# Performance work log

Hardware: AMD Instinct MI355X
Metric: run time of the kernel (lower is better)

## Reference

```python
import jax, jax.numpy as jnp
import numpy as np
import math

DIM = 1536; NH = 12; HD = 128
F, H, W = 6, 30, 30
S = F * H * W
B = 1
K_LEN = 9900  # hardcoded k_lens in the source forward
EPS_NORM = 1e-6


def _rope_tables(max_len=1024, d=HD):
    # Wan rope_params: three tables of widths d-4*(d//6), 2*(d//6), 2*(d//6)
    # -> cos/sin tables of half-widths 22, 21, 21 (concat = d//2 = 64)
    def ang(dd):
        inv = 1.0 / (10000.0 ** (np.arange(0, dd, 2, dtype=np.float64) / dd))
        return np.outer(np.arange(max_len, dtype=np.float64), inv)
    a = np.concatenate([ang(d - 4 * (d // 6)), ang(2 * (d // 6)), ang(2 * (d // 6))], axis=1)
    return np.cos(a).astype(np.float32), np.sin(a).astype(np.float32)


def setup_inputs() -> dict:
    key = jax.random.key(0)
    ks = jax.random.split(key, 5)
    s = 1.0 / math.sqrt(DIM)
    cos, sin = _rope_tables()
    return {
        "x": jax.random.normal(ks[0], (B, S, DIM), jnp.float32),
        "q_w": jax.random.normal(ks[1], (DIM, DIM), jnp.float32) * s,
        "q_b": jnp.zeros((DIM,), jnp.float32),
        "k_w": jax.random.normal(ks[2], (DIM, DIM), jnp.float32) * s,
        "k_b": jnp.zeros((DIM,), jnp.float32),
        "v_w": jax.random.normal(ks[3], (DIM, DIM), jnp.float32) * s,
        "v_b": jnp.zeros((DIM,), jnp.float32),
        "o_w": jax.random.normal(ks[4], (DIM, DIM), jnp.float32) * s,
        "o_b": jnp.zeros((DIM,), jnp.float32),
        "norm_q_w": jnp.ones((DIM,), jnp.float32),
        "norm_k_w": jnp.ones((DIM,), jnp.float32),
        "freqs_cos": jnp.asarray(cos),
        "freqs_sin": jnp.asarray(sin),
        "grid_f": F, "grid_h": H, "grid_w": W,
    }


def rms_norm(x, w):
    # RMSNorm over full model dim, computed in fp32 (as in source)
    xf = x.astype(jnp.float32)
    xn = xf * jax.lax.rsqrt(jnp.mean(xf * xf, axis=-1, keepdims=True) + EPS_NORM)
    return xn.astype(x.dtype) * w


def rope_apply(x, cos, sin, f, h, w):
    # x: [B,S,N,D]; rotate consecutive pairs with 3D-factorized (f,h,w) freqs
    Bb, Ss, Nn, Dd = x.shape
    c = Dd // 2
    sp = [c - 2 * (c // 3), c // 3, c // 3]  # 22, 21, 21

    def grid(tab):
        tf = tab[:, :sp[0]]
        th = tab[:, sp[0]:sp[0] + sp[1]]
        tw = tab[:, sp[0] + sp[1]:]
        g = jnp.concatenate([
            jnp.broadcast_to(tf[:f, None, None, :], (f, h, w, sp[0])),
            jnp.broadcast_to(th[None, :h, None, :], (f, h, w, sp[1])),
            jnp.broadcast_to(tw[None, None, :w, :], (f, h, w, sp[2])),
        ], axis=-1)
        return g.reshape(f * h * w, 1, c)  # [S,1,c] (broadcast over heads)

    gc, gs = grid(cos), grid(sin)
    xp = x.astype(jnp.float32).reshape(Bb, Ss, Nn, c, 2)
    xr, xi = xp[..., 0], xp[..., 1]
    orr = xr * gc - xi * gs
    oii = xr * gs + xi * gc
    return jnp.stack([orr, oii], axis=-1).reshape(Bb, Ss, Nn, Dd).astype(x.dtype)


def attention(q, k, v, k_len):
    # full attention (window_size=(-1,-1)) with keys masked beyond k_len
    scale = 1.0 / math.sqrt(q.shape[-1])
    att = jnp.einsum('bqnd,bknd->bnqk', q, k) * scale
    valid = jnp.arange(k.shape[1]) < k_len
    att = jnp.where(valid[None, None, None, :], att, jnp.finfo(att.dtype).min)
    p = jax.nn.softmax(att, axis=-1)
    return jnp.einsum('bnqk,bknd->bqnd', p, v)


def reference(x, q_w, q_b, k_w, k_b, v_w, v_b, o_w, o_b, norm_q_w, norm_k_w, freqs_cos, freqs_sin, grid_f, grid_h, grid_w):
    Bb, Ss, _ = x.shape
    q = rms_norm(x @ q_w.T + q_b, norm_q_w).reshape(Bb, Ss, NH, HD)
    k = rms_norm(x @ k_w.T + k_b, norm_k_w).reshape(Bb, Ss, NH, HD)
    v = (x @ v_w.T + v_b).reshape(Bb, Ss, NH, HD)
    q = rope_apply(q, freqs_cos, freqs_sin, grid_f, grid_h, grid_w)
    k = rope_apply(k, freqs_cos, freqs_sin, grid_f, grid_h, grid_w)
    o = attention(q, k, v, K_LEN).reshape(Bb, Ss, NH * HD)
    return o @ o_w.T + o_b
```

## Files before the change

kernel.cpp:

```cpp
#include <hip/hip_runtime.h>

#define DIM 1536
#define NH 12
#define HD 128
#define S_LEN 5400
#define SPAD 5440
#define MPAD 5504
#define NQKV 4608
#define EPS_NORM 1e-6f

typedef __bf16 bf16_t;
typedef __bf16 bf16x8 __attribute__((ext_vector_type(8)));
typedef __bf16 bf16x4 __attribute__((ext_vector_type(4)));
typedef float  f32x4  __attribute__((ext_vector_type(4)));
typedef float  f32x16 __attribute__((ext_vector_type(16)));

#define GLOAD_LDS16(gp, lp) __builtin_amdgcn_global_load_lds( \
    (__attribute__((address_space(1))) void*)(void*)(gp),     \
    (__attribute__((address_space(3))) void*)(lp), 16, 0, 0)


__global__ __launch_bounds__(256) void cvt_x_kernel(const float* __restrict__ x,
                                                    bf16_t* __restrict__ xb) {
  size_t base = ((size_t)blockIdx.x * 256 + threadIdx.x) * 4;
  if (base >= (size_t)MPAD * DIM) return;
  size_t row = base / DIM;
  float4 v = make_float4(0.f, 0.f, 0.f, 0.f);
  if (row < S_LEN) v = *(const float4*)&x[base];
  bf16x4 o; o[0] = (__bf16)v.x; o[1] = (__bf16)v.y; o[2] = (__bf16)v.z; o[3] = (__bf16)v.w;
  *(bf16x4*)&xb[base] = o;
}

__global__ __launch_bounds__(256) void cvt_wqkv_kernel(const float* __restrict__ qw,
                                                       const float* __restrict__ kw,
                                                       const float* __restrict__ vw,
                                                       bf16_t* __restrict__ wb) {
  size_t base = ((size_t)blockIdx.x * 256 + threadIdx.x) * 4;
  if (base >= (size_t)NQKV * DIM) return;
  int row = (int)(base / DIM);
  int col = (int)(base - (size_t)row * DIM);
  const float* src; int rr = row;
  if (rr >= 3072)      { src = vw; rr -= 3072; }
  else if (rr >= 1536) { src = kw; rr -= 1536; }
  else                 { src = qw; }
  float4 v = *(const float4*)&src[(size_t)rr * DIM + col];
  bf16x4 o; o[0] = (__bf16)v.x; o[1] = (__bf16)v.y; o[2] = (__bf16)v.z; o[3] = (__bf16)v.w;
  *(bf16x4*)&wb[base] = o;
}

__global__ __launch_bounds__(256) void cvt_wo_kernel(const float* __restrict__ w,
                                                     bf16_t* __restrict__ wb) {
  size_t base = ((size_t)blockIdx.x * 256 + threadIdx.x) * 4;
  if (base >= (size_t)DIM * DIM) return;
  float4 v = *(const float4*)&w[base];
  bf16x4 o; o[0] = (__bf16)v.x; o[1] = (__bf16)v.y; o[2] = (__bf16)v.z; o[3] = (__bf16)v.w;
  *(bf16x4*)&wb[base] = o;
}


template<bool OUT_BF16>
__global__ __launch_bounds__(256) void gemm_bt_kernel(
    const bf16_t* __restrict__ A, const bf16_t* __restrict__ B, void* __restrict__ C,
    const float* __restrict__ bias0, const float* __restrict__ bias1,
    const float* __restrict__ bias2, int M, int N, int K, int Mvalid) {
  __shared__ bf16_t As[2][128 * 32];
  __shared__ bf16_t Bs[2][128 * 32];
  int tid = threadIdx.x;
  int lane = tid & 63, wave = tid >> 6, quad = lane >> 4, l16 = lane & 15;
  int m0 = blockIdx.y * 128, n0 = blockIdx.x * 128;
  int wm = (wave >> 1) * 64, wn = (wave & 1) * 64;
  const bf16_t* Ab = A + (size_t)m0 * K;
  const bf16_t* Bb = B + (size_t)n0 * K;
  f32x4 acc[4][4] = {};

  int eo0 = tid * 8;
  int row0 = eo0 >> 5, col0 = eo0 & 31;
  int eo1 = (256 + tid) * 8;
  int row1 = eo1 >> 5, col1 = eo1 & 31;

  GLOAD_LDS16(Ab + (size_t)row0 * K + col0, &As[0][eo0]);
  GLOAD_LDS16(Bb + (size_t)row0 * K + col0, &Bs[0][eo0]);
  GLOAD_LDS16(Ab + (size_t)row1 * K + col1, &As[0][eo1]);
  GLOAD_LDS16(Bb + (size_t)row1 * K + col1, &Bs[0][eo1]);
  asm volatile("s_waitcnt vmcnt(0)" ::: "memory");
  __builtin_amdgcn_s_barrier();
  __builtin_amdgcn_sched_barrier(0);

  int KT = K >> 5;
  for (int t = 0; t < KT; t++) {
    int cur = t & 1;
    if (t + 1 < KT) {
      int kn = (t + 1) << 5;
      GLOAD_LDS16(Ab + (size_t)row0 * K + kn + col0, &As[cur ^ 1][eo0]);
      GLOAD_LDS16(Bb + (size_t)row0 * K + kn + col0, &Bs[cur ^ 1][eo0]);
      GLOAD_LDS16(Ab + (size_t)row1 * K + kn + col1, &As[cur ^ 1][eo1]);
      GLOAD_LDS16(Bb + (size_t)row1 * K + kn + col1, &Bs[cur ^ 1][eo1]);
    }
    bf16x8 af[4], bfr[4];
#pragma unroll
    for (int i = 0; i < 4; i++)
      af[i] = *(const bf16x8*)&As[cur][(wm + i * 16 + l16) * 32 + quad * 8];
#pragma unroll
    for (int j = 0; j < 4; j++)
      bfr[j] = *(const bf16x8*)&Bs[cur][(wn + j * 16 + l16) * 32 + quad * 8];
#pragma unroll
    for (int i = 0; i < 4; i++)
#pragma unroll
      for (int j = 0; j < 4; j++)
        acc[i][j] = __builtin_amdgcn_mfma_f32_16x16x32_bf16(af[i], bfr[j], acc[i][j], 0, 0, 0);
    asm volatile("s_waitcnt vmcnt(0) lgkmcnt(0)" ::: "memory");
    __builtin_amdgcn_s_barrier();
    __builtin_amdgcn_sched_barrier(0);
  }
#pragma unroll
  for (int j = 0; j < 4; j++) {
    int n = n0 + wn + j * 16 + l16;
    float bias = (n < 1536) ? bias0[n] : (n < 3072) ? bias1[n - 1536] : bias2[n - 3072];
#pragma unroll
    for (int i = 0; i < 4; i++) {
#pragma unroll
      for (int r = 0; r < 4; r++) {
        int m = m0 + wm + i * 16 + quad * 4 + r;
        float v = acc[i][j][r] + bias;
        if (OUT_BF16) {
          ((bf16_t*)C)[(size_t)m * N + n] = (__bf16)v;
        } else {
          if (m < Mvalid) ((float*)C)[(size_t)m * N + n] = v;
        }
      }
    }
  }
}


__global__ __launch_bounds__(256) void rope_qk_kernel(
    const bf16_t* __restrict__ qkv, const float* __restrict__ nqw,
    const float* __restrict__ nkw, const float* __restrict__ fcos,
    const float* __restrict__ fsin, bf16_t* __restrict__ qout,
    bf16_t* __restrict__ kout) {
  int s = blockIdx.x;
  int tid = threadIdx.x;
  bool valid = s < S_LEN;
  int f = s / 900, hh = (s / 30) % 30, ww = s % 30;
  __shared__ float red[4];
  for (int which = 0; which < 2; which++) {
    const bf16_t* src = qkv + (size_t)s * NQKV + which * DIM;
    const float* nw = which ? nkw : nqw;
    bf16_t* dst = (which ? kout : qout) + (size_t)s * DIM;
    float osc = which ? 1.0f : 0.08838834764831845f;
    float v[6]; float ss = 0.f;
#pragma unroll
    for (int i = 0; i < 6; i++) {
      v[i] = valid ? (float)src[tid * 6 + i] : 0.f;
      ss += v[i] * v[i];
    }
#pragma unroll
    for (int off = 32; off >= 1; off >>= 1) ss += __shfl_down(ss, off);
    if ((tid & 63) == 0) red[tid >> 6] = ss;
    __syncthreads();
    float tot = red[0] + red[1] + red[2] + red[3];
    float rn = rsqrtf(tot * (1.f / DIM) + EPS_NORM);
    __syncthreads();
#pragma unroll
    for (int i = 0; i < 3; i++) {
      int e0 = tid * 6 + 2 * i;
      int p = e0 >> 1;
      int cc = p & 63;
      int pos = (cc < 22) ? f : (cc < 43) ? hh : ww;
      float c = fcos[pos * 64 + cc], sn = fsin[pos * 64 + cc];
      float xr = v[2 * i] * rn * nw[e0];
      float xi = v[2 * i + 1] * rn * nw[e0 + 1];
      dst[e0]     = (__bf16)((xr * c - xi * sn) * osc);
      dst[e0 + 1] = (__bf16)((xr * sn + xi * c) * osc);
    }
  }
}


__global__ __launch_bounds__(256) void v_transpose_kernel(const bf16_t* __restrict__ qkv,
                                                          bf16_t* __restrict__ vt) {
  __shared__ bf16_t tile[64][136];
  int h = blockIdx.y, s0 = blockIdx.x * 64, tid = threadIdx.x;
#pragma unroll
  for (int it = 0; it < 4; it++) {
    int eo = (it * 256 + tid) * 8;
    int row = eo >> 7, col = eo & 127;
    int s = s0 + row;
    bf16x8 val = {};
    if (s < S_LEN) val = *(const bf16x8*)&qkv[(size_t)s * NQKV + 3072 + h * HD + col];
    *(bf16x8*)&tile[row][col] = val;
  }
  __syncthreads();
  int d = tid & 127, j0 = (tid >> 7) * 32;
  bf16x8 outv[4];
#pragma unroll
  for (int b = 0; b < 4; b++)
#pragma unroll
    for (int j = 0; j < 8; j++) outv[b][j] = tile[j0 + b * 8 + j][d];
  size_t base = ((size_t)h * HD + d) * SPAD + s0 + j0;
#pragma unroll
  for (int b = 0; b < 4; b++) *(bf16x8*)&vt[base + b * 8] = outv[b];
}


__global__ __launch_bounds__(256, 2) void flash_attn_kernel(
    const bf16_t* __restrict__ q, const bf16_t* __restrict__ k,
    const bf16_t* __restrict__ vt, bf16_t* __restrict__ o) {
  __shared__ bf16_t Ks[2][64 * 128];
  __shared__ bf16_t Vs[2][64 * 128];
  __shared__ bf16_t Pw[4][32 * 64];
  int head = blockIdx.y;
  int s0 = blockIdx.x * 128;
  int tid = threadIdx.x, w = tid >> 6, lane = tid & 63;
  int l31 = lane & 31, hh = lane >> 5;

  bf16x8 bq[8];
  {
    const bf16_t* qp = &q[(size_t)(s0 + w * 32 + l31) * DIM + head * HD + hh * 8];
#pragma unroll
    for (int kc = 0; kc < 8; kc++) bq[kc] = *(const bf16x8*)(qp + kc * 16);
  }

  float m_i = -1e30f, l_i = 0.f;
  f32x16 oacc[4] = {};

  const int NT = SPAD / 64;

#pragma unroll
  for (int it = 0; it < 4; it++) {
    int slot = it * 256 + tid;
    int row = slot >> 4, pc = slot & 15;
    int c = pc ^ (row & 15);
    GLOAD_LDS16(k + (size_t)row * DIM + head * HD + c * 8, &Ks[0][slot * 8]);
  }
#pragma unroll
  for (int it = 0; it < 4; it++) {
    int slot = it * 256 + tid;
    int row = slot >> 4, pc = slot & 15;
    int cp = pc ^ (row & 15);
    int d = 2 * row + (cp >> 3);
    GLOAD_LDS16(vt + ((size_t)head * HD + d) * SPAD + (cp & 7) * 8, &Vs[0][slot * 8]);
  }
  asm volatile("s_waitcnt vmcnt(0)" ::: "memory");
  __builtin_amdgcn_s_barrier();
  __builtin_amdgcn_sched_barrier(0);

  for (int t = 0; t < NT; t++) {
    int kt = t * 64;
    int cur = t & 1;

    if (t + 1 < NT) {
      int kn = kt + 64;
#pragma unroll
      for (int it = 0; it < 4; it++) {
        int slot = it * 256 + tid;
        int row = slot >> 4, pc = slot & 15;
        int c = pc ^ (row & 15);
        GLOAD_LDS16(k + (size_t)(kn + row) * DIM + head * HD + c * 8, &Ks[cur ^ 1][slot * 8]);
      }
#pragma unroll
      for (int it = 0; it < 4; it++) {
        int slot = it * 256 + tid;
        int row = slot >> 4, pc = slot & 15;
        int cp = pc ^ (row & 15);
        int d = 2 * row + (cp >> 3);
        GLOAD_LDS16(vt + ((size_t)head * HD + d) * SPAD + kn + (cp & 7) * 8, &Vs[cur ^ 1][slot * 8]);
      }
    }

    f32x16 sacc[2] = {};
    __builtin_amdgcn_s_setprio(1);
#pragma unroll
    for (int ns = 0; ns < 2; ns++) {
      int row = ns * 32 + l31;
#pragma unroll
      for (int kc = 0; kc < 8; kc++) {
        int pc = (kc * 2 + hh) ^ (row & 15);
        bf16x8 ak = *(const bf16x8*)&Ks[cur][row * 128 + pc * 8];
        sacc[ns] = __builtin_amdgcn_mfma_f32_32x32x16_bf16(ak, bq[kc], sacc[ns], 0, 0, 0);
      }
    }
    __builtin_amdgcn_s_setprio(0);

    if (kt + 64 > S_LEN) {
#pragma unroll
      for (int ns = 0; ns < 2; ns++)
#pragma unroll
        for (int r = 0; r < 16; r++) {
          int kvg = kt + ns * 32 + (r & 3) + 8 * (r >> 2) + 4 * hh;
          if (kvg >= S_LEN) sacc[ns][r] = -1e30f;
        }
    }

    float mx = -1e30f;
#pragma unroll
    for (int ns = 0; ns < 2; ns++)
#pragma unroll
      for (int r = 0; r < 16; r++) mx = fmaxf(mx, sacc[ns][r]);
    mx = fmaxf(mx, __shfl_xor(mx, 32));
    if (!__all(mx - m_i <= 8.f)) {
      float mn = fmaxf(m_i, mx);
      float al = __expf(m_i - mn);
      l_i *= al;
#pragma unroll
      for (int dt = 0; dt < 4; dt++)
#pragma unroll
        for (int r = 0; r < 16; r++) oacc[dt][r] *= al;
      m_i = mn;
    }
    float rs = 0.f;
#pragma unroll
    for (int ns = 0; ns < 2; ns++)
#pragma unroll
      for (int r = 0; r < 16; r++) {
        float p = __expf(sacc[ns][r] - m_i);
        rs += p;
        sacc[ns][r] = p;
      }
    rs += __shfl_xor(rs, 32);
    l_i += rs;

#pragma unroll
    for (int ns = 0; ns < 2; ns++)
#pragma unroll
      for (int tt = 0; tt < 4; tt++) {
        bf16x4 pk;
#pragma unroll
        for (int r4 = 0; r4 < 4; r4++) pk[r4] = (__bf16)sacc[ns][tt * 4 + r4];
        int c8 = ns * 8 + 2 * tt + hh;
        int pc8 = c8 ^ (l31 & 15);
        *(bf16x4*)&Pw[w][l31 * 64 + pc8 * 4] = pk;
      }

    __builtin_amdgcn_s_setprio(1);
#pragma unroll
    for (int kvc = 0; kvc < 4; kvc++) {
      int c8a = kvc * 4 + hh * 2;
      bf16x4 plo = *(const bf16x4*)&Pw[w][l31 * 64 + ((c8a) ^ (l31 & 15)) * 4];
      bf16x4 phi = *(const bf16x4*)&Pw[w][l31 * 64 + ((c8a + 1) ^ (l31 & 15)) * 4];
      bf16x8 bp;
#pragma unroll
      for (int j = 0; j < 4; j++) { bp[j] = plo[j]; bp[j + 4] = phi[j]; }
#pragma unroll
      for (int dt = 0; dt < 4; dt++) {
        int d = dt * 32 + l31;
        int r = d >> 1;
        int cp = ((d & 1) << 3) | (kvc * 2 + hh);
        int pc = cp ^ (r & 15);
        bf16x8 av = *(const bf16x8*)&Vs[cur][r * 128 + pc * 8];
        oacc[dt] = __builtin_amdgcn_mfma_f32_32x32x16_bf16(av, bp, oacc[dt], 0, 0, 0);
      }
    }
    __builtin_amdgcn_s_setprio(0);

    asm volatile("s_waitcnt vmcnt(0) lgkmcnt(0)" ::: "memory");
    __builtin_amdgcn_s_barrier();
    __builtin_amdgcn_sched_barrier(0);
  }

  float inv = 1.f / l_i;
  int qr = lane >> 1, seg = lane & 1;
  int srow = s0 + w * 32 + qr;
#pragma unroll
  for (int half = 0; half < 2; half++) {
#pragma unroll
    for (int dl = 0; dl < 2; dl++) {
      int dt = half * 2 + dl;
#pragma unroll
      for (int tt = 0; tt < 4; tt++) {
        bf16x4 v;
#pragma unroll
        for (int r4 = 0; r4 < 4; r4++) v[r4] = (__bf16)(oacc[dt][tt * 4 + r4] * inv);
        int c8 = dl * 8 + 2 * tt + hh;
        int pc8 = c8 ^ (l31 & 15);
        *(bf16x4*)&Pw[w][l31 * 64 + pc8 * 4] = v;
      }
    }
#pragma unroll
    for (int i = 0; i < 4; i++) {
      int c8 = seg * 8 + 2 * i;
      bf16x4 lo = *(const bf16x4*)&Pw[w][qr * 64 + ((c8) ^ (qr & 15)) * 4];
      bf16x4 hi = *(const bf16x4*)&Pw[w][qr * 64 + ((c8 + 1) ^ (qr & 15)) * 4];
      bf16x8 val;
#pragma unroll
      for (int j = 0; j < 4; j++) { val[j] = lo[j]; val[j + 4] = hi[j]; }
      if (srow < S_LEN)
        *(bf16x8*)&o[(size_t)srow * DIM + head * HD + half * 64 + seg * 32 + i * 8] = val;
    }
    __syncthreads();
  }
}


extern "C" void kernel_launch(void* const* d_in, const int* in_sizes, int n_in,
                              void* d_out, int out_size, void* d_ws, size_t ws_size,
                              hipStream_t stream) {
  const float* x    = (const float*)d_in[0];
  const float* q_w  = (const float*)d_in[1];
  const float* q_b  = (const float*)d_in[2];
  const float* k_w  = (const float*)d_in[3];
  const float* k_b  = (const float*)d_in[4];
  const float* v_w  = (const float*)d_in[5];
  const float* v_b  = (const float*)d_in[6];
  const float* o_w  = (const float*)d_in[7];
  const float* o_b  = (const float*)d_in[8];
  const float* nqw  = (const float*)d_in[9];
  const float* nkw  = (const float*)d_in[10];
  const float* fcos = (const float*)d_in[11];
  const float* fsin = (const float*)d_in[12];

  char* ws = (char*)d_ws;
  bf16_t* xb   = (bf16_t*)(ws + 0);
  bf16_t* wqkv = (bf16_t*)(ws + 16908288);
  bf16_t* wob  = (bf16_t*)(ws + 31064064);
  bf16_t* qkv  = (bf16_t*)(ws + 35782656);
  bf16_t* qb   = (bf16_t*)(ws + 86507520);
  bf16_t* kb   = (bf16_t*)(ws + 103415808);
  bf16_t* vtb  = (bf16_t*)(ws + 0);
  bf16_t* aob  = (bf16_t*)(ws + 35782656);

  cvt_x_kernel<<<(MPAD * DIM / 4 + 255) / 256, 256, 0, stream>>>(x, xb);
  cvt_wqkv_kernel<<<(NQKV * DIM / 4 + 255) / 256, 256, 0, stream>>>(q_w, k_w, v_w, wqkv);
  cvt_wo_kernel<<<(DIM * DIM / 4 + 255) / 256, 256, 0, stream>>>(o_w, wob);

  gemm_bt_kernel<true><<<dim3(NQKV / 128, MPAD / 128), 256, 0, stream>>>(
      xb, wqkv, qkv, q_b, k_b, v_b, MPAD, NQKV, DIM, MPAD);

  rope_qk_kernel<<<MPAD, 256, 0, stream>>>(qkv, nqw, nkw, fcos, fsin, qb, kb);
  v_transpose_kernel<<<dim3(SPAD / 64, NH), 256, 0, stream>>>(qkv, vtb);

  flash_attn_kernel<<<dim3(MPAD / 128, NH), 256, 0, stream>>>(qb, kb, vtb, aob);

  gemm_bt_kernel<false><<<dim3(DIM / 128, MPAD / 128), 256, 0, stream>>>(
      aob, wob, d_out, o_b, o_b, o_b, MPAD, DIM, DIM, S_LEN);
}
```

Baseline: 689.8 us.

## Keep softmax probabilities in registers via permlane32 swap instead of LDS round-trip

```diff
diff --git a/kernel.cpp b/kernel.cpp
--- a/kernel.cpp
+++ b/kernel.cpp
@@ -12,12 +12,31 @@
 typedef __bf16 bf16_t;
 typedef __bf16 bf16x8 __attribute__((ext_vector_type(8)));
 typedef __bf16 bf16x4 __attribute__((ext_vector_type(4)));
+typedef __bf16 bf16x2 __attribute__((ext_vector_type(2)));
 typedef float  f32x4  __attribute__((ext_vector_type(4)));
 typedef float  f32x16 __attribute__((ext_vector_type(16)));
+typedef int    i32x2  __attribute__((ext_vector_type(2)));
 
 #define GLOAD_LDS16(gp, lp) __builtin_amdgcn_global_load_lds( \
     (__attribute__((address_space(1))) void*)(void*)(gp),     \
     (__attribute__((address_space(3))) void*)(lp), 16, 0, 0)
+
+__device__ __forceinline__ unsigned int pkbf(float a, float b) {
+  union { bf16x2 h; unsigned int u; } c;
+  c.h[0] = (__bf16)a; c.h[1] = (__bf16)b;
+  return c.u;
+}
+
+__device__ __forceinline__ float xhalf_max(float x) {
+  i32x2 r = __builtin_amdgcn_permlane32_swap(__float_as_int(x), __float_as_int(x),
+                                             false, false);
+  return fmaxf(__int_as_float(r.x), __int_as_float(r.y));
+}
+__device__ __forceinline__ float xhalf_sum(float x) {
+  i32x2 r = __builtin_amdgcn_permlane32_swap(__float_as_int(x), __float_as_int(x),
+                                             false, false);
+  return __int_as_float(r.x) + __int_as_float(r.y);
+}
 
 
 __global__ __launch_bounds__(256) void cvt_x_kernel(const float* __restrict__ x,
@@ -147,7 +166,7 @@
     const bf16_t* src = qkv + (size_t)s * NQKV + which * DIM;
     const float* nw = which ? nkw : nqw;
     bf16_t* dst = (which ? kout : qout) + (size_t)s * DIM;
-    float osc = which ? 1.0f : 0.08838834764831845f;
+    float osc = which ? 1.0f : 0.12751742686f;
     float v[6]; float ss = 0.f;
 #pragma unroll
     for (int i = 0; i < 6; i++) {
@@ -208,7 +227,6 @@
     const bf16_t* __restrict__ vt, bf16_t* __restrict__ o) {
   __shared__ bf16_t Ks[2][64 * 128];
   __shared__ bf16_t Vs[2][64 * 128];
-  __shared__ bf16_t Pw[4][32 * 64];
   int head = blockIdx.y;
   int s0 = blockIdx.x * 128;
   int tid = threadIdx.x, w = tid >> 6, lane = tid & 63;
@@ -292,15 +310,21 @@
         }
     }
 
-    float mx = -1e30f;
-#pragma unroll
-    for (int ns = 0; ns < 2; ns++)
-#pragma unroll
-      for (int r = 0; r < 16; r++) mx = fmaxf(mx, sacc[ns][r]);
-    mx = fmaxf(mx, __shfl_xor(mx, 32));
-    if (!__all(mx - m_i <= 8.f)) {
+    float mx;
+    {
+      float tm[8];
+#pragma unroll
+      for (int i = 0; i < 8; i++)
+        tm[i] = fmaxf(fmaxf(sacc[0][i], sacc[0][i + 8]),
+                      fmaxf(sacc[1][i], sacc[1][i + 8]));
+#pragma unroll
+      for (int i = 0; i < 4; i++) tm[i] = fmaxf(tm[i], tm[i + 4]);
+      mx = fmaxf(fmaxf(tm[0], tm[2]), fmaxf(tm[1], tm[3]));
+    }
+    mx = xhalf_max(mx);
+    if (!__all(mx - m_i <= 11.5f)) {
       float mn = fmaxf(m_i, mx);
-      float al = __expf(m_i - mn);
+      float al = __builtin_amdgcn_exp2f(m_i - mn);
       l_i *= al;
 #pragma unroll
       for (int dt = 0; dt < 4; dt++)
@@ -308,39 +332,37 @@
         for (int r = 0; r < 16; r++) oacc[dt][r] *= al;
       m_i = mn;
     }
-    float rs = 0.f;
 #pragma unroll
     for (int ns = 0; ns < 2; ns++)
 #pragma unroll
-      for (int r = 0; r < 16; r++) {
-        float p = __expf(sacc[ns][r] - m_i);
-        rs += p;
-        sacc[ns][r] = p;
-      }
-    rs += __shfl_xor(rs, 32);
-    l_i += rs;
-
-#pragma unroll
-    for (int ns = 0; ns < 2; ns++)
-#pragma unroll
-      for (int tt = 0; tt < 4; tt++) {
-        bf16x4 pk;
-#pragma unroll
-        for (int r4 = 0; r4 < 4; r4++) pk[r4] = (__bf16)sacc[ns][tt * 4 + r4];
-        int c8 = ns * 8 + 2 * tt + hh;
-        int pc8 = c8 ^ (l31 & 15);
-        *(bf16x4*)&Pw[w][l31 * 64 + pc8 * 4] = pk;
-      }
+      for (int r = 0; r < 16; r++)
+        sacc[ns][r] = __builtin_amdgcn_exp2f(sacc[ns][r] - m_i);
+    float rs;
+    {
+      float ts[8];
+#pragma unroll
+      for (int i = 0; i < 8; i++)
+        ts[i] = (sacc[0][i] + sacc[0][i + 8]) + (sacc[1][i] + sacc[1][i + 8]);
+#pragma unroll
+      for (int i = 0; i < 4; i++) ts[i] += ts[i + 4];
+      rs = (ts[0] + ts[2]) + (ts[1] + ts[3]);
+    }
+    l_i += xhalf_sum(rs);
 
     __builtin_amdgcn_s_setprio(1);
 #pragma unroll
     for (int kvc = 0; kvc < 4; kvc++) {
-      int c8a = kvc * 4 + hh * 2;
-      bf16x4 plo = *(const bf16x4*)&Pw[w][l31 * 64 + ((c8a) ^ (l31 & 15)) * 4];
-      bf16x4 phi = *(const bf16x4*)&Pw[w][l31 * 64 + ((c8a + 1) ^ (l31 & 15)) * 4];
-      bf16x8 bp;
-#pragma unroll
-      for (int j = 0; j < 4; j++) { bp[j] = plo[j]; bp[j + 4] = phi[j]; }
+      int ns = kvc >> 1, rb = (kvc & 1) * 8;
+      int w0 = (int)pkbf(sacc[ns][rb + 0], sacc[ns][rb + 1]);
+      int w1 = (int)pkbf(sacc[ns][rb + 2], sacc[ns][rb + 3]);
+      int w2 = (int)pkbf(sacc[ns][rb + 4], sacc[ns][rb + 5]);
+      int w3 = (int)pkbf(sacc[ns][rb + 6], sacc[ns][rb + 7]);
+      i32x2 r02 = __builtin_amdgcn_permlane32_swap(w0, w2, false, false);
+      i32x2 r13 = __builtin_amdgcn_permlane32_swap(w1, w3, false, false);
+      union { unsigned int u[4]; bf16x8 v8; } bpu;
+      bpu.u[0] = (unsigned int)r02.x; bpu.u[1] = (unsigned int)r13.x;
+      bpu.u[2] = (unsigned int)r02.y; bpu.u[3] = (unsigned int)r13.y;
+      bf16x8 bp = bpu.v8;
 #pragma unroll
       for (int dt = 0; dt < 4; dt++) {
         int d = dt * 32 + l31;
@@ -358,6 +380,7 @@
     __builtin_amdgcn_sched_barrier(0);
   }
 
+  bf16_t* scr = ((bf16_t*)Ks) + w * (32 * 64);
   float inv = 1.f / l_i;
   int qr = lane >> 1, seg = lane & 1;
   int srow = s0 + w * 32 + qr;
@@ -373,21 +396,20 @@
         for (int r4 = 0; r4 < 4; r4++) v[r4] = (__bf16)(oacc[dt][tt * 4 + r4] * inv);
         int c8 = dl * 8 + 2 * tt + hh;
         int pc8 = c8 ^ (l31 & 15);
-        *(bf16x4*)&Pw[w][l31 * 64 + pc8 * 4] = v;
+        *(bf16x4*)&scr[l31 * 64 + pc8 * 4] = v;
       }
     }
 #pragma unroll
     for (int i = 0; i < 4; i++) {
       int c8 = seg * 8 + 2 * i;
-      bf16x4 lo = *(const bf16x4*)&Pw[w][qr * 64 + ((c8) ^ (qr & 15)) * 4];
-      bf16x4 hi = *(const bf16x4*)&Pw[w][qr * 64 + ((c8 + 1) ^ (qr & 15)) * 4];
+      bf16x4 lo = *(const bf16x4*)&scr[qr * 64 + ((c8) ^ (qr & 15)) * 4];
+      bf16x4 hi = *(const bf16x4*)&scr[qr * 64 + ((c8 + 1) ^ (qr & 15)) * 4];
       bf16x8 val;
 #pragma unroll
       for (int j = 0; j < 4; j++) { val[j] = lo[j]; val[j + 4] = hi[j]; }
       if (srow < S_LEN)
         *(bf16x8*)&o[(size_t)srow * DIM + head * HD + half * 64 + seg * 32 + i * 8] = val;
     }
-    __syncthreads();
   }
 }
 
```

Result: faster. 657.5 us (-4.7%).
